# Optimization experiments

Hardware: AMD Instinct MI355X
Metric: run time of the kernel (lower is better)

## Reference

```python
import jax, jax.numpy as jnp
import numpy as np

D_MODEL = 1024
NHEAD = 16
HEAD_DIM = D_MODEL // NHEAD
SF_THRESHOLD = 4.0
SF_LEVELS = 8
SF_STEP = SF_THRESHOLD / SF_LEVELS  # 0.5
EPS = 1e-6


def sfn(x):
    # Scale-and-Fire neuron: quantize activations to multiples of SF_STEP,
    # clipped to +/- num_levels, with straight-through estimator.
    q = jnp.clip(jnp.round(x / SF_STEP), -SF_LEVELS, SF_LEVELS) * SF_STEP
    return x + jax.lax.stop_gradient(q - x)


def qk_norm(x, g):
    # RMS-normalize over the head_dim (last axis) with learnable gain g [Dh].
    rms = jnp.sqrt(jnp.mean(x * x, axis=-1, keepdims=True) + EPS)
    return (x / rms) * g


def setup_inputs() -> dict:
    key = jax.random.key(0)
    ks = jax.random.split(key, 10)
    B, L, D = 2, 2048, D_MODEL
    s = 1.0 / np.sqrt(D)
    return {
        "x": jax.random.normal(ks[0], (B, L, D), dtype=jnp.float32),
        "Wq": jax.random.normal(ks[1], (D, D), dtype=jnp.float32) * s,
        "bq": jnp.zeros((D,), dtype=jnp.float32),
        "Wk": jax.random.normal(ks[2], (D, D), dtype=jnp.float32) * s,
        "bk": jnp.zeros((D,), dtype=jnp.float32),
        "Wv": jax.random.normal(ks[3], (D, D), dtype=jnp.float32) * s,
        "bv": jnp.zeros((D,), dtype=jnp.float32),
        "Wo": jax.random.normal(ks[4], (D, D), dtype=jnp.float32) * s,
        "bo": jnp.zeros((D,), dtype=jnp.float32),
        "gq": jnp.ones((HEAD_DIM,), dtype=jnp.float32),
        "gk": jnp.ones((HEAD_DIM,), dtype=jnp.float32),
    }


def reference(x, Wq, bq, Wk, bk, Wv, bv, Wo, bo, gq, gk):
    B, L, D = x.shape
    H, Dh = NHEAD, HEAD_DIM
    scale = Dh ** (-0.5)

    q = sfn(x @ Wq.T + bq)
    k = sfn(x @ Wk.T + bk)
    v = sfn(x @ Wv.T + bv)

    # [B, L, H, Dh] -> [B, H, L, Dh]
    q = q.reshape(B, L, H, Dh).transpose(0, 2, 1, 3)
    k = k.reshape(B, L, H, Dh).transpose(0, 2, 1, 3)
    v = v.reshape(B, L, H, Dh).transpose(0, 2, 1, 3)

    q = qk_norm(q, gq)
    k = qk_norm(k, gk)

    scores = jnp.einsum('bhqd,bhkd->bhqk', q, k) * scale
    probs = jax.nn.softmax(scores, axis=-1)  # dropout is identity (eval)
    out = jnp.einsum('bhqk,bhkd->bhqd', probs, v)
    out = out.transpose(0, 2, 1, 3).reshape(B, L, D)
    return out @ Wo.T + bo
```

## Files before the change

kernel.cpp:

```cpp
#include <hip/hip_runtime.h>
#include <math.h>


typedef __bf16 bf16;
typedef bf16 bf16x4 __attribute__((ext_vector_type(4)));
typedef bf16 bf16x8 __attribute__((ext_vector_type(8)));
typedef float f32x4 __attribute__((ext_vector_type(4)));

#define LOG2E 1.4426950408889634f

__device__ __forceinline__ float sfn_f(float x) {
  return fminf(fmaxf(rintf(x + x), -8.0f), 8.0f) * 0.5f;
}

__device__ __forceinline__ void gload16(const bf16* g, bf16* l) {
  __builtin_amdgcn_global_load_lds((const __attribute__((address_space(1))) void*)g,
                                   (__attribute__((address_space(3))) void*)l, 16, 0, 0);
}


__global__ __launch_bounds__(256) void prep_x_kernel(const float* __restrict__ x,
                                                     bf16* __restrict__ ax) {
  int idx = blockIdx.x * 256 + threadIdx.x;
  int m  = idx >> 8;
  int kc = (idx & 255) << 2;
  const float4 v = *(const float4*)(x + (size_t)m * 1024 + kc);
  bf16 h0 = (bf16)v.x, h1 = (bf16)v.y, h2 = (bf16)v.z, h3 = (bf16)v.w;
  bf16 l0 = (bf16)(v.x - (float)h0), l1 = (bf16)(v.y - (float)h1),
       l2 = (bf16)(v.z - (float)h2), l3 = (bf16)(v.w - (float)h3);
  bf16x4 hv = {h0, h1, h2, h3};
  bf16x4 lv = {l0, l1, l2, l3};
  bf16* p = ax + (size_t)m * 3072 + kc;
  *(bf16x4*)(p)        = hv;
  *(bf16x4*)(p + 1024) = lv;
  *(bf16x4*)(p + 2048) = hv;
}

__global__ __launch_bounds__(256) void prep_w_kernel(const float* __restrict__ Wq,
                                                     const float* __restrict__ Wk,
                                                     const float* __restrict__ Wv,
                                                     bf16* __restrict__ wc) {
  int idx = blockIdx.x * 256 + threadIdx.x;
  int mat = idx >> 18;
  int r   = idx & 262143;
  int n   = r >> 8;
  int kc  = (r & 255) << 2;
  const float* W = (mat == 0) ? Wq : ((mat == 1) ? Wk : Wv);
  const float4 v = *(const float4*)(W + (size_t)n * 1024 + kc);
  bf16 h0 = (bf16)v.x, h1 = (bf16)v.y, h2 = (bf16)v.z, h3 = (bf16)v.w;
  bf16 l0 = (bf16)(v.x - (float)h0), l1 = (bf16)(v.y - (float)h1),
       l2 = (bf16)(v.z - (float)h2), l3 = (bf16)(v.w - (float)h3);
  bf16x4 hv = {h0, h1, h2, h3};
  bf16x4 lv = {l0, l1, l2, l3};
  bf16* p = wc + (size_t)(mat * 1024 + n) * 3072 + kc;
  *(bf16x4*)(p)        = hv;
  *(bf16x4*)(p + 1024) = hv;
  *(bf16x4*)(p + 2048) = lv;
}

__global__ __launch_bounds__(256) void prep_wo_kernel(const float* __restrict__ Wo,
                                                      bf16* __restrict__ wob) {
  int idx = blockIdx.x * 256 + threadIdx.x;
  const float4 v = *(const float4*)(Wo + (size_t)idx * 4);
  bf16x4 hv = {(bf16)v.x, (bf16)v.y, (bf16)v.z, (bf16)v.w};
  *(bf16x4*)(wob + (size_t)idx * 4) = hv;
}


template <int MODE>
__global__ __launch_bounds__(256, 3) void gemm_bt_kernel(
    const bf16* __restrict__ A, const bf16* __restrict__ Bm, int K,
    const float* __restrict__ b0, const float* __restrict__ b1,
    const float* __restrict__ b2, const float* __restrict__ g0,
    const float* __restrict__ g1, bf16* __restrict__ qn, bf16* __restrict__ kn,
    bf16* __restrict__ vt, float* __restrict__ outf) {
  __shared__ bf16 sA[128 * 32];
  __shared__ bf16 sB[128 * 32];
  const int tid  = threadIdx.x;
  const int wave = tid >> 6;
  const int lane = tid & 63;
  const int lm   = lane & 15;
  const int kg   = lane >> 4;
  const int nbx = gridDim.x;
  const int lid = blockIdx.x + nbx * blockIdx.y;
  const int cpx = (nbx << 5) >> 3;
  const int logical = (lid & 7) * cpx + (lid >> 3);
  const int m0 = (logical / nbx) << 7;
  const int n0 = (logical % nbx) << 7;
  const int wm = (wave >> 1) << 6;
  const int wn = (wave & 1) << 6;

  f32x4 acc[4][4] = {};

  for (int kt = 0; kt < K; kt += 32) {
    __syncthreads();
#pragma unroll
    for (int j = 0; j < 2; ++j) {
      const int i   = wave * 128 + j * 64 + lane;
      const int row = i >> 2;
      const int kc  = (i & 3) << 3;
      gload16(A  + (size_t)(m0 + row) * K + kt + kc, sA + i * 8);
      gload16(Bm + (size_t)(n0 + row) * K + kt + kc, sB + i * 8);
    }
    __syncthreads();
    bf16x8 af[4], bfv[4];
#pragma unroll
    for (int r = 0; r < 4; ++r)
      af[r] = *(const bf16x8*)(sA + (wm + 16 * r + lm) * 32 + kg * 8);
#pragma unroll
    for (int c = 0; c < 4; ++c)
      bfv[c] = *(const bf16x8*)(sB + (wn + 16 * c + lm) * 32 + kg * 8);
#pragma unroll
    for (int r = 0; r < 4; ++r)
#pragma unroll
      for (int c = 0; c < 4; ++c)
        acc[r][c] = __builtin_amdgcn_mfma_f32_16x16x32_bf16(af[r], bfv[c], acc[r][c], 0, 0, 0);
  }

  if (MODE == 0) {
    const int ncb = n0 + wn;
    const int mat = ncb >> 10;
    const int nin = ncb & 1023;
    const int hh  = nin >> 6;
    const float* bias = (mat == 0) ? b0 : ((mat == 1) ? b1 : b2);
    float bvals[4];
#pragma unroll
    for (int c = 0; c < 4; ++c) bvals[c] = bias[nin + 16 * c + lm];

    if (mat < 2) {
      const float* gain = (mat == 0) ? g0 : g1;
      bf16* dst = (mat == 0) ? qn : kn;
      float gv[4];
#pragma unroll
      for (int c = 0; c < 4; ++c) gv[c] = gain[16 * c + lm];
#pragma unroll
      for (int r = 0; r < 4; ++r) {
        float y[4][4];
        float ss[4] = {0.f, 0.f, 0.f, 0.f};
#pragma unroll
        for (int c = 0; c < 4; ++c)
#pragma unroll
          for (int g = 0; g < 4; ++g) {
            float t = sfn_f(acc[r][c][g] + bvals[c]);
            y[c][g] = t;
            ss[g] += t * t;
          }
#pragma unroll
        for (int g = 0; g < 4; ++g) {
          float s = ss[g];
          s += __shfl_xor(s, 1);
          s += __shfl_xor(s, 2);
          s += __shfl_xor(s, 4);
          s += __shfl_xor(s, 8);
          ss[g] = 1.0f / sqrtf(s * (1.0f / 64.0f) + 1e-6f);
        }
        const int mbase = m0 + wm + 16 * r + 4 * kg;
        const int bb = mbase >> 11;
        const int ll = mbase & 2047;
#pragma unroll
        for (int g = 0; g < 4; ++g) {
          bf16* rowp = dst + ((size_t)(bb * 16 + hh) * 2048 + (ll + g)) * 64;
#pragma unroll
          for (int c = 0; c < 4; ++c)
            rowp[16 * c + lm] = (bf16)(y[c][g] * ss[g] * gv[c]);
        }
      }
    } else {
#pragma unroll
      for (int r = 0; r < 4; ++r) {
        const int mbase = m0 + wm + 16 * r + 4 * kg;
        const int bb = mbase >> 11;
        const int ll = mbase & 2047;
#pragma unroll
        for (int c = 0; c < 4; ++c) {
          bf16x4 pk;
#pragma unroll
          for (int g = 0; g < 4; ++g)
            pk[g] = (bf16)sfn_f(acc[r][c][g] + bvals[c]);
          *(bf16x4*)(vt + ((size_t)(bb * 16 + hh) * 64 + 16 * c + lm) * 2048 + ll) = pk;
        }
      }
    }
  } else {
    float bvals[4];
#pragma unroll
    for (int c = 0; c < 4; ++c) bvals[c] = b0[n0 + wn + 16 * c + lm];
#pragma unroll
    for (int r = 0; r < 4; ++r) {
      const int mr = m0 + wm + 16 * r + 4 * kg;
#pragma unroll
      for (int c = 0; c < 4; ++c) {
        const int nc = n0 + wn + 16 * c + lm;
#pragma unroll
        for (int g = 0; g < 4; ++g)
          outf[(size_t)(mr + g) * 1024 + nc] = acc[r][c][g] + bvals[c];
      }
    }
  }
}


__global__ __launch_bounds__(256, 3) void attn_kernel(const bf16* __restrict__ qn,
                                                      const bf16* __restrict__ kn,
                                                      const bf16* __restrict__ vt,
                                                      bf16* __restrict__ ao) {
  __shared__ bf16 sK[2][64 * 64];
  __shared__ bf16 sV[2][64 * 64];
  __shared__ bf16 sP[4][16 * 72];
  const int tid  = threadIdx.x;
  const int wave = tid >> 6;
  const int lane = tid & 63;
  const int lm   = lane & 15;
  const int kg   = lane >> 4;
  const int lid     = blockIdx.x + (blockIdx.y << 4);
  const int logical = ((lid & 7) << 6) | (lid >> 3);
  const int qblk    = logical & 15;
  const int bh      = logical >> 4;
  const int q0      = (qblk << 7) + (wave << 5);
  const bf16* qb = qn + (size_t)bh * 2048 * 64;
  const bf16* kb = kn + (size_t)bh * 2048 * 64;
  const bf16* vb = vt + (size_t)bh * 64 * 2048;

  const float C1 = 0.125f * LOG2E;
  const float C2 = -8.0f * LOG2E;

  const int srow7 = lane >> 3;
  const int scl   = (lane & 7) ^ srow7;
  auto stage = [&](int buf, int kt) {
#pragma unroll
    for (int j = 0; j < 2; ++j) {
      const int ci  = wave * 2 + j;
      const int row = ci * 8 + srow7;
      gload16(kb + (size_t)(kt + row) * 64 + scl * 8, &sK[buf][ci * 512]);
      gload16(vb + (size_t)row * 2048 + kt + scl * 8, &sV[buf][ci * 512]);
    }
  };

  bf16x8 qf[2][2];
#pragma unroll
  for (int c = 0; c < 2; ++c)
#pragma unroll
    for (int dh = 0; dh < 2; ++dh)
      qf[c][dh] = *(const bf16x8*)(qb + (size_t)(q0 + 16 * c + lm) * 64 + dh * 32 + kg * 8);

  f32x4 o[4][2] = {};
  float lrun[2] = {0.f, 0.f};

  stage(0, 0);
  asm volatile("s_waitcnt vmcnt(0)" ::: "memory");
  __syncthreads();

  const int a7 = lm & 7;
  for (int t = 0; t < 32; ++t) {
    const int cur = t & 1;
    if (t < 31) stage(cur ^ 1, (t + 1) * 64);

    bf16x8 ka[4][2];
#pragma unroll
    for (int rb = 0; rb < 4; ++rb)
#pragma unroll
      for (int dh = 0; dh < 2; ++dh)
        ka[rb][dh] = *(const bf16x8*)(&sK[cur][(16 * rb + lm) * 64 + ((dh * 4 + kg) ^ a7) * 8]);

    f32x4 s[4][2] = {};
#pragma unroll
    for (int rb = 0; rb < 4; ++rb)
#pragma unroll
      for (int c = 0; c < 2; ++c)
#pragma unroll
        for (int dh = 0; dh < 2; ++dh)
          s[rb][c] = __builtin_amdgcn_mfma_f32_16x16x32_bf16(ka[rb][dh], qf[c][dh], s[rb][c], 0, 0, 0);

    bf16x8 pb[2][2];
#pragma unroll
    for (int c = 0; c < 2; ++c) {
#pragma unroll
      for (int rb = 0; rb < 4; ++rb) {
        bf16x4 pk;
#pragma unroll
        for (int g = 0; g < 4; ++g) {
          float p = __builtin_amdgcn_exp2f(fmaf(s[rb][c][g], C1, C2));
          lrun[c] += p;
          pk[g] = (bf16)p;
        }
        *(bf16x4*)(&sP[wave][lm * 72 + 16 * rb + 4 * kg]) = pk;
      }
      asm volatile("s_waitcnt lgkmcnt(0)" ::: "memory");
#pragma unroll
      for (int kh = 0; kh < 2; ++kh)
        pb[c][kh] = *(const bf16x8*)(&sP[wave][lm * 72 + kh * 32 + kg * 8]);
    }

    bf16x8 va[4][2];
#pragma unroll
    for (int rbd = 0; rbd < 4; ++rbd)
#pragma unroll
      for (int kh = 0; kh < 2; ++kh)
        va[rbd][kh] = *(const bf16x8*)(&sV[cur][(16 * rbd + lm) * 64 + ((kh * 4 + kg) ^ a7) * 8]);

#pragma unroll
    for (int rbd = 0; rbd < 4; ++rbd)
#pragma unroll
      for (int c = 0; c < 2; ++c)
#pragma unroll
        for (int kh = 0; kh < 2; ++kh)
          o[rbd][c] = __builtin_amdgcn_mfma_f32_16x16x32_bf16(va[rbd][kh], pb[c][kh], o[rbd][c], 0, 0, 0);

    asm volatile("s_waitcnt vmcnt(0)" ::: "memory");
    __syncthreads();
  }

  const int bb = bh >> 4;
  const int hh = bh & 15;
#pragma unroll
  for (int c = 0; c < 2; ++c) {
    float l = lrun[c];
    l += __shfl_xor(l, 16);
    l += __shfl_xor(l, 32);
    const float inv = 1.0f / l;
    const int q = q0 + 16 * c + lm;
    bf16* rowp = ao + (size_t)(bb * 2048 + q) * 1024 + hh * 64;
#pragma unroll
    for (int rbd = 0; rbd < 4; ++rbd) {
      bf16x4 pk;
#pragma unroll
      for (int g = 0; g < 4; ++g)
        pk[g] = (bf16)(o[rbd][c][g] * inv);
      *(bf16x4*)(rowp + 16 * rbd + 4 * kg) = pk;
    }
  }
}


extern "C" void kernel_launch(void* const* d_in, const int* in_sizes, int n_in,
                              void* d_out, int out_size, void* d_ws, size_t ws_size,
                              hipStream_t stream) {
  const float* x  = (const float*)d_in[0];
  const float* Wq = (const float*)d_in[1];
  const float* bq = (const float*)d_in[2];
  const float* Wk = (const float*)d_in[3];
  const float* bk = (const float*)d_in[4];
  const float* Wv = (const float*)d_in[5];
  const float* bv = (const float*)d_in[6];
  const float* Wo = (const float*)d_in[7];
  const float* bo = (const float*)d_in[8];
  const float* gq = (const float*)d_in[9];
  const float* gk = (const float*)d_in[10];
  float* out = (float*)d_out;

  char* ws = (char*)d_ws;
  bf16* ax   = (bf16*)(ws);
  bf16* wc   = (bf16*)(ws + 25165824);
  bf16* wob  = (bf16*)(ws + 44040192);
  bf16* qn   = (bf16*)(ws + 46137344);
  bf16* kn   = (bf16*)(ws + 54525952);
  bf16* vt   = (bf16*)(ws + 62914560);
  bf16* attn = (bf16*)(ws + 71303168);

  prep_x_kernel<<<dim3(4096), dim3(256), 0, stream>>>(x, ax);
  prep_w_kernel<<<dim3(3072), dim3(256), 0, stream>>>(Wq, Wk, Wv, wc);
  prep_wo_kernel<<<dim3(1024), dim3(256), 0, stream>>>(Wo, wob);

  gemm_bt_kernel<0><<<dim3(24, 32), dim3(256), 0, stream>>>(
      ax, wc, 3072, bq, bk, bv, gq, gk, qn, kn, vt, nullptr);

  attn_kernel<<<dim3(16, 32), dim3(256), 0, stream>>>(qn, kn, vt, attn);

  gemm_bt_kernel<1><<<dim3(8, 32), dim3(256), 0, stream>>>(
      attn, wob, 1024, bo, nullptr, nullptr, nullptr, nullptr,
      nullptr, nullptr, nullptr, out);
}
```

Measured before the change: 271.9 us.

## Rewrite QKV GEMM as 256x256 pipelined 8-wave kernel and split attention K/V staging

Replaces the QKV projection GEMM with a dedicated 512-thread kernel using 256x256 tiles and K=64 steps. It uses swizzled LDS, staggered half-tile prefetch with partial vmcnt waits, barrier-phased MFMA blocks and setprio. In attention, K and V loads are issued separately so V for the next tile streams in during the current QK step. P also gets a per-column buffer, which drops an intermediate lgkmcnt wait. The goal is more data reuse and better overlap of global loads with MFMA, at the cost of more LDS, more registers and fewer resident blocks.

```diff
diff --git a/kernel.cpp b/kernel.cpp
--- a/kernel.cpp
+++ b/kernel.cpp
@@ -8,6 +8,14 @@
 typedef float f32x4 __attribute__((ext_vector_type(4)));
 
 #define LOG2E 1.4426950408889634f
+#define MFMA16 __builtin_amdgcn_mfma_f32_16x16x32_bf16
+#define S_WAITV(N) asm volatile("s_waitcnt vmcnt(" #N ")" ::: "memory")
+
+__device__ __forceinline__ void bar() {
+  asm volatile("" ::: "memory");
+  __builtin_amdgcn_s_barrier();
+  asm volatile("" ::: "memory");
+}
 
 __device__ __forceinline__ float sfn_f(float x) {
   return fminf(fmaxf(rintf(x + x), -8.0f), 8.0f) * 0.5f;
@@ -67,13 +75,202 @@
 }
 
 
-template <int MODE>
-__global__ __launch_bounds__(256, 3) void gemm_bt_kernel(
-    const bf16* __restrict__ A, const bf16* __restrict__ Bm, int K,
+__global__ __launch_bounds__(512, 2) void gemm_qkv_kernel(
+    const bf16* __restrict__ A, const bf16* __restrict__ Bm,
     const float* __restrict__ b0, const float* __restrict__ b1,
     const float* __restrict__ b2, const float* __restrict__ g0,
     const float* __restrict__ g1, bf16* __restrict__ qn, bf16* __restrict__ kn,
-    bf16* __restrict__ vt, float* __restrict__ outf) {
+    bf16* __restrict__ vt) {
+  constexpr int K = 3072, NT = 48;
+  __shared__ bf16 lds[2][4][128 * 64];
+  const int tid  = threadIdx.x;
+  const int wave = tid >> 6;
+  const int lane = tid & 63;
+  const int lm   = lane & 15;
+  const int kg   = lane >> 4;
+  const int wm   = wave >> 2;
+  const int wn   = wave & 3;
+  const int lid     = blockIdx.x;
+  const int logical = (lid & 7) * 24 + (lid >> 3);
+  const int m0 = (logical / 12) << 8;
+  const int n0 = (logical % 12) << 8;
+
+  const bf16* Abase = A  + (size_t)m0 * K;
+  const bf16* Bbase = Bm + (size_t)n0 * K;
+
+  auto stageHalf = [&](int buf, int half, const bf16* base, int kt) {
+#pragma unroll
+    for (int j = 0; j < 2; ++j) {
+      const int c    = j * 512 + tid;
+      const int row  = c >> 3;
+      const int col8 = (c & 7) ^ (row & 7);
+      gload16(base + (size_t)row * K + kt + col8 * 8, &lds[buf][half][c * 8]);
+    }
+  };
+
+  f32x4 acc[8][4] = {};
+  const int bHalf = 2 + (wn >> 1);
+  const int bRow  = (wn & 1) << 6;
+  const int sw    = lm & 7;
+
+  stageHalf(0, 0, Abase, 0);
+  stageHalf(0, 1, Abase + (size_t)128 * K, 0);
+  stageHalf(0, 2, Bbase, 0);
+  stageHalf(0, 3, Bbase + (size_t)128 * K, 0);
+  stageHalf(1, 0, Abase, 64);
+  stageHalf(1, 1, Abase + (size_t)128 * K, 64);
+  S_WAITV(4);
+  bar();
+
+  for (int t = 0; t < NT; ++t) {
+    const int cur = t & 1, nxt = cur ^ 1;
+    const int kt1 = (t + 1) << 6;
+    bf16x8 a[4][2], p01[2][2], p23[2][2];
+#pragma unroll
+    for (int r = 0; r < 4; ++r)
+#pragma unroll
+      for (int kk = 0; kk < 2; ++kk)
+        a[r][kk] = *(const bf16x8*)&lds[cur][wm][(16 * r + lm) * 64 + (((kk << 2) + kg) ^ sw) * 8];
+#pragma unroll
+    for (int c = 0; c < 2; ++c)
+#pragma unroll
+      for (int kk = 0; kk < 2; ++kk)
+        p01[c][kk] = *(const bf16x8*)&lds[cur][bHalf][(bRow + 16 * c + lm) * 64 + (((kk << 2) + kg) ^ sw) * 8];
+    if (t + 1 < NT) stageHalf(nxt, 2, Bbase, kt1);
+    bar();
+    __builtin_amdgcn_s_setprio(1);
+#pragma unroll
+    for (int r = 0; r < 4; ++r)
+#pragma unroll
+      for (int c = 0; c < 2; ++c)
+#pragma unroll
+        for (int kk = 0; kk < 2; ++kk)
+          acc[r][c] = MFMA16(a[r][kk], p01[c][kk], acc[r][c], 0, 0, 0);
+    __builtin_amdgcn_s_setprio(0);
+    bar();
+#pragma unroll
+    for (int c = 0; c < 2; ++c)
+#pragma unroll
+      for (int kk = 0; kk < 2; ++kk)
+        p23[c][kk] = *(const bf16x8*)&lds[cur][bHalf][(bRow + 16 * (c + 2) + lm) * 64 + (((kk << 2) + kg) ^ sw) * 8];
+    if (t + 1 < NT) stageHalf(nxt, 3, Bbase + (size_t)128 * K, kt1);
+    bar();
+    __builtin_amdgcn_s_setprio(1);
+#pragma unroll
+    for (int r = 0; r < 4; ++r)
+#pragma unroll
+      for (int c = 0; c < 2; ++c)
+#pragma unroll
+        for (int kk = 0; kk < 2; ++kk)
+          acc[r][c + 2] = MFMA16(a[r][kk], p23[c][kk], acc[r][c + 2], 0, 0, 0);
+    __builtin_amdgcn_s_setprio(0);
+    bar();
+#pragma unroll
+    for (int r = 0; r < 4; ++r)
+#pragma unroll
+      for (int kk = 0; kk < 2; ++kk)
+        a[r][kk] = *(const bf16x8*)&lds[cur][wm][(64 + 16 * r + lm) * 64 + (((kk << 2) + kg) ^ sw) * 8];
+    bar();
+    __builtin_amdgcn_s_setprio(1);
+#pragma unroll
+    for (int r = 0; r < 4; ++r)
+#pragma unroll
+      for (int c = 0; c < 2; ++c)
+#pragma unroll
+        for (int kk = 0; kk < 2; ++kk)
+          acc[4 + r][c + 2] = MFMA16(a[r][kk], p23[c][kk], acc[4 + r][c + 2], 0, 0, 0);
+    __builtin_amdgcn_s_setprio(0);
+    bar();
+    if (t + 2 < NT) {
+      const int kt2 = (t + 2) << 6;
+      stageHalf(cur, 0, Abase, kt2);
+      stageHalf(cur, 1, Abase + (size_t)128 * K, kt2);
+      S_WAITV(4);
+    } else {
+      S_WAITV(0);
+    }
+    bar();
+    __builtin_amdgcn_s_setprio(1);
+#pragma unroll
+    for (int r = 0; r < 4; ++r)
+#pragma unroll
+      for (int c = 0; c < 2; ++c)
+#pragma unroll
+        for (int kk = 0; kk < 2; ++kk)
+          acc[4 + r][c] = MFMA16(a[r][kk], p01[c][kk], acc[4 + r][c], 0, 0, 0);
+    __builtin_amdgcn_s_setprio(0);
+    bar();
+  }
+
+  const int ncb = n0 + (wn << 6);
+  const int mat = ncb >> 10;
+  const int nin = ncb & 1023;
+  const int hh  = nin >> 6;
+  const float* bias = (mat == 0) ? b0 : ((mat == 1) ? b1 : b2);
+  float bvals[4];
+#pragma unroll
+  for (int c = 0; c < 4; ++c) bvals[c] = bias[nin + 16 * c + lm];
+
+  if (mat < 2) {
+    const float* gain = (mat == 0) ? g0 : g1;
+    bf16* dst = (mat == 0) ? qn : kn;
+    float gv[4];
+#pragma unroll
+    for (int c = 0; c < 4; ++c) gv[c] = gain[16 * c + lm];
+#pragma unroll
+    for (int r = 0; r < 8; ++r) {
+      float y[4][4];
+      float ss[4] = {0.f, 0.f, 0.f, 0.f};
+#pragma unroll
+      for (int c = 0; c < 4; ++c)
+#pragma unroll
+        for (int g = 0; g < 4; ++g) {
+          float tq = sfn_f(acc[r][c][g] + bvals[c]);
+          y[c][g] = tq;
+          ss[g] += tq * tq;
+        }
+#pragma unroll
+      for (int g = 0; g < 4; ++g) {
+        float s = ss[g];
+        s += __shfl_xor(s, 1);
+        s += __shfl_xor(s, 2);
+        s += __shfl_xor(s, 4);
+        s += __shfl_xor(s, 8);
+        ss[g] = 1.0f / sqrtf(s * (1.0f / 64.0f) + 1e-6f);
+      }
+      const int mbase = m0 + (wm << 7) + 16 * r + 4 * kg;
+      const int bb = mbase >> 11;
+      const int ll = mbase & 2047;
+#pragma unroll
+      for (int g = 0; g < 4; ++g) {
+        bf16* rowp = dst + ((size_t)(bb * 16 + hh) * 2048 + (ll + g)) * 64;
+#pragma unroll
+        for (int c = 0; c < 4; ++c)
+          rowp[16 * c + lm] = (bf16)(y[c][g] * ss[g] * gv[c]);
+      }
+    }
+  } else {
+#pragma unroll
+    for (int r = 0; r < 8; ++r) {
+      const int mbase = m0 + (wm << 7) + 16 * r + 4 * kg;
+      const int bb = mbase >> 11;
+      const int ll = mbase & 2047;
+#pragma unroll
+      for (int c = 0; c < 4; ++c) {
+        bf16x4 pk;
+#pragma unroll
+        for (int g = 0; g < 4; ++g)
+          pk[g] = (bf16)sfn_f(acc[r][c][g] + bvals[c]);
+        *(bf16x4*)(vt + ((size_t)(bb * 16 + hh) * 64 + 16 * c + lm) * 2048 + ll) = pk;
+      }
+    }
+  }
+}
+
+
+__global__ __launch_bounds__(256, 3) void gemm_o_kernel(
+    const bf16* __restrict__ A, const bf16* __restrict__ Bm, int K,
+    const float* __restrict__ b0, float* __restrict__ outf) {
   __shared__ bf16 sA[128 * 32];
   __shared__ bf16 sB[128 * 32];
   const int tid  = threadIdx.x;
@@ -114,87 +311,21 @@
     for (int r = 0; r < 4; ++r)
 #pragma unroll
       for (int c = 0; c < 4; ++c)
-        acc[r][c] = __builtin_amdgcn_mfma_f32_16x16x32_bf16(af[r], bfv[c], acc[r][c], 0, 0, 0);
+        acc[r][c] = MFMA16(af[r], bfv[c], acc[r][c], 0, 0, 0);
   }
 
-  if (MODE == 0) {
-    const int ncb = n0 + wn;
-    const int mat = ncb >> 10;
-    const int nin = ncb & 1023;
-    const int hh  = nin >> 6;
-    const float* bias = (mat == 0) ? b0 : ((mat == 1) ? b1 : b2);
-    float bvals[4];
-#pragma unroll
-    for (int c = 0; c < 4; ++c) bvals[c] = bias[nin + 16 * c + lm];
-
-    if (mat < 2) {
-      const float* gain = (mat == 0) ? g0 : g1;
-      bf16* dst = (mat == 0) ? qn : kn;
-      float gv[4];
-#pragma unroll
-      for (int c = 0; c < 4; ++c) gv[c] = gain[16 * c + lm];
-#pragma unroll
-      for (int r = 0; r < 4; ++r) {
-        float y[4][4];
-        float ss[4] = {0.f, 0.f, 0.f, 0.f};
-#pragma unroll
-        for (int c = 0; c < 4; ++c)
-#pragma unroll
-          for (int g = 0; g < 4; ++g) {
-            float t = sfn_f(acc[r][c][g] + bvals[c]);
-            y[c][g] = t;
-            ss[g] += t * t;
-          }
-#pragma unroll
-        for (int g = 0; g < 4; ++g) {
-          float s = ss[g];
-          s += __shfl_xor(s, 1);
-          s += __shfl_xor(s, 2);
-          s += __shfl_xor(s, 4);
-          s += __shfl_xor(s, 8);
-          ss[g] = 1.0f / sqrtf(s * (1.0f / 64.0f) + 1e-6f);
-        }
-        const int mbase = m0 + wm + 16 * r + 4 * kg;
-        const int bb = mbase >> 11;
-        const int ll = mbase & 2047;
-#pragma unroll
-        for (int g = 0; g < 4; ++g) {
-          bf16* rowp = dst + ((size_t)(bb * 16 + hh) * 2048 + (ll + g)) * 64;
-#pragma unroll
-          for (int c = 0; c < 4; ++c)
-            rowp[16 * c + lm] = (bf16)(y[c][g] * ss[g] * gv[c]);
-        }
-      }
-    } else {
-#pragma unroll
-      for (int r = 0; r < 4; ++r) {
-        const int mbase = m0 + wm + 16 * r + 4 * kg;
-        const int bb = mbase >> 11;
-        const int ll = mbase & 2047;
-#pragma unroll
-        for (int c = 0; c < 4; ++c) {
-          bf16x4 pk;
-#pragma unroll
-          for (int g = 0; g < 4; ++g)
-            pk[g] = (bf16)sfn_f(acc[r][c][g] + bvals[c]);
-          *(bf16x4*)(vt + ((size_t)(bb * 16 + hh) * 64 + 16 * c + lm) * 2048 + ll) = pk;
-        }
-      }
-    }
-  } else {
-    float bvals[4];
-#pragma unroll
-    for (int c = 0; c < 4; ++c) bvals[c] = b0[n0 + wn + 16 * c + lm];
-#pragma unroll
-    for (int r = 0; r < 4; ++r) {
-      const int mr = m0 + wm + 16 * r + 4 * kg;
-#pragma unroll
-      for (int c = 0; c < 4; ++c) {
-        const int nc = n0 + wn + 16 * c + lm;
-#pragma unroll
-        for (int g = 0; g < 4; ++g)
-          outf[(size_t)(mr + g) * 1024 + nc] = acc[r][c][g] + bvals[c];
-      }
+  float bvals[4];
+#pragma unroll
+  for (int c = 0; c < 4; ++c) bvals[c] = b0[n0 + wn + 16 * c + lm];
+#pragma unroll
+  for (int r = 0; r < 4; ++r) {
+    const int mr = m0 + wm + 16 * r + 4 * kg;
+#pragma unroll
+    for (int c = 0; c < 4; ++c) {
+      const int nc = n0 + wn + 16 * c + lm;
+#pragma unroll
+      for (int g = 0; g < 4; ++g)
+        outf[(size_t)(mr + g) * 1024 + nc] = acc[r][c][g] + bvals[c];
     }
   }
 }
@@ -206,7 +337,7 @@
                                                       bf16* __restrict__ ao) {
   __shared__ bf16 sK[2][64 * 64];
   __shared__ bf16 sV[2][64 * 64];
-  __shared__ bf16 sP[4][16 * 72];
+  __shared__ bf16 sP[4][2][16 * 72];
   const int tid  = threadIdx.x;
   const int wave = tid >> 6;
   const int lane = tid & 63;
@@ -226,12 +357,19 @@
 
   const int srow7 = lane >> 3;
   const int scl   = (lane & 7) ^ srow7;
-  auto stage = [&](int buf, int kt) {
+  auto stageK = [&](int buf, int kt) {
 #pragma unroll
     for (int j = 0; j < 2; ++j) {
       const int ci  = wave * 2 + j;
       const int row = ci * 8 + srow7;
       gload16(kb + (size_t)(kt + row) * 64 + scl * 8, &sK[buf][ci * 512]);
+    }
+  };
+  auto stageV = [&](int buf, int kt) {
+#pragma unroll
+    for (int j = 0; j < 2; ++j) {
+      const int ci  = wave * 2 + j;
+      const int row = ci * 8 + srow7;
       gload16(vb + (size_t)row * 2048 + kt + scl * 8, &sV[buf][ci * 512]);
     }
   };
@@ -246,14 +384,16 @@
   f32x4 o[4][2] = {};
   float lrun[2] = {0.f, 0.f};
 
-  stage(0, 0);
-  asm volatile("s_waitcnt vmcnt(0)" ::: "memory");
-  __syncthreads();
+  stageK(0, 0);
+  stageV(0, 0);
+  S_WAITV(0);
+  bar();
 
   const int a7 = lm & 7;
   for (int t = 0; t < 32; ++t) {
-    const int cur = t & 1;
-    if (t < 31) stage(cur ^ 1, (t + 1) * 64);
+    const int cur = t & 1, nxt = cur ^ 1;
+    const int ktn = (t + 1) << 6;
+    if (t < 31) stageK(nxt, ktn);
 
     bf16x8 ka[4][2];
 #pragma unroll
@@ -263,17 +403,20 @@
         ka[rb][dh] = *(const bf16x8*)(&sK[cur][(16 * rb + lm) * 64 + ((dh * 4 + kg) ^ a7) * 8]);
 
     f32x4 s[4][2] = {};
+    __builtin_amdgcn_s_setprio(1);
 #pragma unroll
     for (int rb = 0; rb < 4; ++rb)
 #pragma unroll
       for (int c = 0; c < 2; ++c)
 #pragma unroll
         for (int dh = 0; dh < 2; ++dh)
-          s[rb][c] = __builtin_amdgcn_mfma_f32_16x16x32_bf16(ka[rb][dh], qf[c][dh], s[rb][c], 0, 0, 0);
-
-    bf16x8 pb[2][2];
-#pragma unroll
-    for (int c = 0; c < 2; ++c) {
+          s[rb][c] = MFMA16(ka[rb][dh], qf[c][dh], s[rb][c], 0, 0, 0);
+    __builtin_amdgcn_s_setprio(0);
+
+    if (t < 31) stageV(nxt, ktn);
+
+#pragma unroll
+    for (int c = 0; c < 2; ++c)
 #pragma unroll
       for (int rb = 0; rb < 4; ++rb) {
         bf16x4 pk;
@@ -283,13 +426,17 @@
           lrun[c] += p;
           pk[g] = (bf16)p;
         }
-        *(bf16x4*)(&sP[wave][lm * 72 + 16 * rb + 4 * kg]) = pk;
+        *(bf16x4*)(&sP[wave][c][lm * 72 + 16 * rb + 4 * kg]) = pk;
       }
-      asm volatile("s_waitcnt lgkmcnt(0)" ::: "memory");
+    bf16x8 pb[2][2];
+#pragma unroll
+    for (int c = 0; c < 2; ++c)
 #pragma unroll
       for (int kh = 0; kh < 2; ++kh)
-        pb[c][kh] = *(const bf16x8*)(&sP[wave][lm * 72 + kh * 32 + kg * 8]);
-    }
+        pb[c][kh] = *(const bf16x8*)(&sP[wave][c][lm * 72 + kh * 32 + kg * 8]);
+
+    if (t < 31) { S_WAITV(4); } else { S_WAITV(0); }
+    bar();
 
     bf16x8 va[4][2];
 #pragma unroll
@@ -298,16 +445,20 @@
       for (int kh = 0; kh < 2; ++kh)
         va[rbd][kh] = *(const bf16x8*)(&sV[cur][(16 * rbd + lm) * 64 + ((kh * 4 + kg) ^ a7) * 8]);
 
+    __builtin_amdgcn_s_setprio(1);
 #pragma unroll
     for (int rbd = 0; rbd < 4; ++rbd)
 #pragma unroll
       for (int c = 0; c < 2; ++c)
 #pragma unroll
         for (int kh = 0; kh < 2; ++kh)
-          o[rbd][c] = __builtin_amdgcn_mfma_f32_16x16x32_bf16(va[rbd][kh], pb[c][kh], o[rbd][c], 0, 0, 0);
-
-    asm volatile("s_waitcnt vmcnt(0)" ::: "memory");
-    __syncthreads();
+          o[rbd][c] = MFMA16(va[rbd][kh], pb[c][kh], o[rbd][c], 0, 0, 0);
+    __builtin_amdgcn_s_setprio(0);
+
+    if (t < 31) {
+      S_WAITV(2);
+      bar();
+    }
   }
 
   const int bb = bh >> 4;
@@ -361,12 +512,11 @@
   prep_w_kernel<<<dim3(3072), dim3(256), 0, stream>>>(Wq, Wk, Wv, wc);
   prep_wo_kernel<<<dim3(1024), dim3(256), 0, stream>>>(Wo, wob);
 
-  gemm_bt_kernel<0><<<dim3(24, 32), dim3(256), 0, stream>>>(
-      ax, wc, 3072, bq, bk, bv, gq, gk, qn, kn, vt, nullptr);
+  gemm_qkv_kernel<<<dim3(192), dim3(512), 0, stream>>>(
+      ax, wc, bq, bk, bv, gq, gk, qn, kn, vt);
 
   attn_kernel<<<dim3(16, 32), dim3(256), 0, stream>>>(qn, kn, vt, attn);
 
-  gemm_bt_kernel<1><<<dim3(8, 32), dim3(256), 0, stream>>>(
-      attn, wob, 1024, bo, nullptr, nullptr, nullptr, nullptr,
-      nullptr, nullptr, nullptr, out);
-}
+  gemm_o_kernel<<<dim3(8, 32), dim3(256), 0, stream>>>(
+      attn, wob, 1024, bo, out);
+}
```

New measurement: 260.4 us. 1.04x faster.

## Retile QKV GEMM to 256x192 with 12 waves and load attention K/V into registers

Applied to the files above, without the earlier changes.

The fused QKV projection GEMM moves to a dedicated kernel with 768-thread blocks and 256x192 output tiles. It uses a K-step of 64, XOR-swizzled LDS double buffering and s_setprio around MFMA bursts. This raises operand reuse per LDS load and cuts the block count to one wave of 256 blocks. The attention kernel drops LDS staging of K/V and loads them straight from global memory into registers, ping-ponging two tiles to overlap loads with MFMA. That removes barriers but adds register pressure, so its occupancy hint falls to 2.

```diff
diff --git a/kernel.cpp b/kernel.cpp
--- a/kernel.cpp
+++ b/kernel.cpp
@@ -8,6 +8,14 @@
 typedef float f32x4 __attribute__((ext_vector_type(4)));
 
 #define LOG2E 1.4426950408889634f
+#define MFMA16 __builtin_amdgcn_mfma_f32_16x16x32_bf16
+#define S_WAITV(N) asm volatile("s_waitcnt vmcnt(" #N ")" ::: "memory")
+
+__device__ __forceinline__ void bar() {
+  asm volatile("" ::: "memory");
+  __builtin_amdgcn_s_barrier();
+  asm volatile("" ::: "memory");
+}
 
 __device__ __forceinline__ float sfn_f(float x) {
   return fminf(fmaxf(rintf(x + x), -8.0f), 8.0f) * 0.5f;
@@ -67,13 +75,163 @@
 }
 
 
-template <int MODE>
-__global__ __launch_bounds__(256, 3) void gemm_bt_kernel(
-    const bf16* __restrict__ A, const bf16* __restrict__ Bm, int K,
+__global__ __launch_bounds__(768, 3) void gemm_qkv_kernel(
+    const bf16* __restrict__ A, const bf16* __restrict__ Bm,
     const float* __restrict__ b0, const float* __restrict__ b1,
     const float* __restrict__ b2, const float* __restrict__ g0,
     const float* __restrict__ g1, bf16* __restrict__ qn, bf16* __restrict__ kn,
-    bf16* __restrict__ vt, float* __restrict__ outf) {
+    bf16* __restrict__ vt) {
+  constexpr int K = 3072, NT = 48;
+  __shared__ bf16 lds[2][3584 * 8];
+  const int tid  = threadIdx.x;
+  const int wave = tid >> 6;
+  const int lane = tid & 63;
+  const int lm   = lane & 15;
+  const int kg   = lane >> 4;
+  const int wmr  = wave & 3;
+  const int wnc  = wave >> 2;
+  const int lid     = blockIdx.x;
+  const int logical = ((lid & 7) << 5) | (lid >> 3);
+  const int m0 = (logical >> 4) << 8;
+  const int n0 = (logical & 15) * 192;
+
+  auto stage = [&](int buf, int kt) {
+#pragma unroll
+    for (int j = 0; j < 5; ++j) {
+      const int i = tid + j * 768;
+      if (i < 3584) {
+        if (i < 2048) {
+          const int row  = i >> 3;
+          const int col8 = (i & 7) ^ (row & 7);
+          gload16(A + (size_t)(m0 + row) * K + kt + col8 * 8, &lds[buf][i * 8]);
+        } else {
+          const int i2   = i - 2048;
+          const int row  = i2 >> 3;
+          const int col8 = (i2 & 7) ^ (row & 7);
+          gload16(Bm + (size_t)(n0 + row) * K + kt + col8 * 8, &lds[buf][i * 8]);
+        }
+      }
+    }
+  };
+
+  auto rdA = [&](int buf, int r, int kk) -> bf16x8 {
+    const int row = (wmr << 6) + (r << 4) + lm;
+    return *(const bf16x8*)&lds[buf][(row * 8 + (((kk << 2) + kg) ^ (row & 7))) * 8];
+  };
+  auto rdB = [&](int buf, int c, int kk) -> bf16x8 {
+    const int row = (wnc << 6) + (c << 4) + lm;
+    return *(const bf16x8*)&lds[buf][(2048 * 8) + (row * 8 + (((kk << 2) + kg) ^ (row & 7))) * 8];
+  };
+
+  f32x4 acc[4][4] = {};
+
+  stage(0, 0);
+  S_WAITV(0);
+  bar();
+
+  for (int t = 0; t < NT; ++t) {
+    const int cur = t & 1;
+    if (t + 1 < NT) stage(cur ^ 1, (t + 1) << 6);
+
+    bf16x8 a0[4], bq0[4];
+#pragma unroll
+    for (int r = 0; r < 4; ++r) a0[r] = rdA(cur, r, 0);
+#pragma unroll
+    for (int c = 0; c < 4; ++c) bq0[c] = rdB(cur, c, 0);
+    __builtin_amdgcn_s_setprio(1);
+#pragma unroll
+    for (int r = 0; r < 4; ++r)
+#pragma unroll
+      for (int c = 0; c < 4; ++c)
+        acc[r][c] = MFMA16(a0[r], bq0[c], acc[r][c], 0, 0, 0);
+    __builtin_amdgcn_s_setprio(0);
+
+    bf16x8 a1[4], bq1[4];
+#pragma unroll
+    for (int r = 0; r < 4; ++r) a1[r] = rdA(cur, r, 1);
+#pragma unroll
+    for (int c = 0; c < 4; ++c) bq1[c] = rdB(cur, c, 1);
+    __builtin_amdgcn_s_setprio(1);
+#pragma unroll
+    for (int r = 0; r < 4; ++r)
+#pragma unroll
+      for (int c = 0; c < 4; ++c)
+        acc[r][c] = MFMA16(a1[r], bq1[c], acc[r][c], 0, 0, 0);
+    __builtin_amdgcn_s_setprio(0);
+
+    S_WAITV(0);
+    bar();
+  }
+
+  const int gcol = n0 + (wnc << 6);
+  const int mat  = gcol >> 10;
+  const int cb   = gcol & 1023;
+  const int hh   = cb >> 6;
+  const float* bias = (mat == 0) ? b0 : ((mat == 1) ? b1 : b2);
+  float bvals[4];
+#pragma unroll
+  for (int j = 0; j < 4; ++j) bvals[j] = bias[cb + 16 * j + lm];
+
+  if (mat < 2) {
+    const float* gain = (mat == 0) ? g0 : g1;
+    bf16* dst = (mat == 0) ? qn : kn;
+    float gv[4];
+#pragma unroll
+    for (int j = 0; j < 4; ++j) gv[j] = gain[16 * j + lm];
+#pragma unroll
+    for (int r = 0; r < 4; ++r) {
+      float y[4][4];
+      float ss[4] = {0.f, 0.f, 0.f, 0.f};
+#pragma unroll
+      for (int j = 0; j < 4; ++j)
+#pragma unroll
+        for (int g = 0; g < 4; ++g) {
+          float tq = sfn_f(acc[r][j][g] + bvals[j]);
+          y[j][g] = tq;
+          ss[g] += tq * tq;
+        }
+#pragma unroll
+      for (int g = 0; g < 4; ++g) {
+        float s = ss[g];
+        s += __shfl_xor(s, 1);
+        s += __shfl_xor(s, 2);
+        s += __shfl_xor(s, 4);
+        s += __shfl_xor(s, 8);
+        ss[g] = 1.0f / sqrtf(s * (1.0f / 64.0f) + 1e-6f);
+      }
+      const int mbase = m0 + (wmr << 6) + 16 * r + 4 * kg;
+      const int bb = mbase >> 11;
+      const int ll = mbase & 2047;
+#pragma unroll
+      for (int g = 0; g < 4; ++g) {
+        bf16* rowp = dst + ((size_t)(bb * 16 + hh) * 2048 + (ll + g)) * 64;
+#pragma unroll
+        for (int j = 0; j < 4; ++j)
+          rowp[16 * j + lm] = (bf16)(y[j][g] * ss[g] * gv[j]);
+      }
+    }
+  } else {
+#pragma unroll
+    for (int r = 0; r < 4; ++r) {
+      const int mbase = m0 + (wmr << 6) + 16 * r + 4 * kg;
+      const int bb = mbase >> 11;
+      const int ll = mbase & 2047;
+#pragma unroll
+      for (int j = 0; j < 4; ++j) {
+        bf16x4 pk;
+#pragma unroll
+        for (int g = 0; g < 4; ++g)
+          pk[g] = (bf16)sfn_f(acc[r][j][g] + bvals[j]);
+        *(bf16x4*)(vt + ((size_t)(bb * 16 + hh) * 64 + 16 * j + lm) * 2048 + ll) = pk;
+      }
+    }
+  }
+}
+
+
+__global__ __launch_bounds__(256, 3) void gemm_o_kernel(
+    const bf16* __restrict__ A, const bf16* __restrict__ Bm, int K,
+    const float* __restrict__ b0, float* __restrict__ outf) {
   __shared__ bf16 sA[128 * 32];
   __shared__ bf16 sB[128 * 32];
   const int tid  = threadIdx.x;
@@ -114,98 +272,30 @@
     for (int r = 0; r < 4; ++r)
 #pragma unroll
       for (int c = 0; c < 4; ++c)
-        acc[r][c] = __builtin_amdgcn_mfma_f32_16x16x32_bf16(af[r], bfv[c], acc[r][c], 0, 0, 0);
-  }
-
-  if (MODE == 0) {
-    const int ncb = n0 + wn;
-    const int mat = ncb >> 10;
-    const int nin = ncb & 1023;
-    const int hh  = nin >> 6;
-    const float* bias = (mat == 0) ? b0 : ((mat == 1) ? b1 : b2);
-    float bvals[4];
-#pragma unroll
-    for (int c = 0; c < 4; ++c) bvals[c] = bias[nin + 16 * c + lm];
-
-    if (mat < 2) {
-      const float* gain = (mat == 0) ? g0 : g1;
-      bf16* dst = (mat == 0) ? qn : kn;
-      float gv[4];
-#pragma unroll
-      for (int c = 0; c < 4; ++c) gv[c] = gain[16 * c + lm];
-#pragma unroll
-      for (int r = 0; r < 4; ++r) {
-        float y[4][4];
-        float ss[4] = {0.f, 0.f, 0.f, 0.f};
-#pragma unroll
-        for (int c = 0; c < 4; ++c)
-#pragma unroll
-          for (int g = 0; g < 4; ++g) {
-            float t = sfn_f(acc[r][c][g] + bvals[c]);
-            y[c][g] = t;
-            ss[g] += t * t;
-          }
-#pragma unroll
-        for (int g = 0; g < 4; ++g) {
-          float s = ss[g];
-          s += __shfl_xor(s, 1);
-          s += __shfl_xor(s, 2);
-          s += __shfl_xor(s, 4);
-          s += __shfl_xor(s, 8);
-          ss[g] = 1.0f / sqrtf(s * (1.0f / 64.0f) + 1e-6f);
-        }
-        const int mbase = m0 + wm + 16 * r + 4 * kg;
-        const int bb = mbase >> 11;
-        const int ll = mbase & 2047;
-#pragma unroll
-        for (int g = 0; g < 4; ++g) {
-          bf16* rowp = dst + ((size_t)(bb * 16 + hh) * 2048 + (ll + g)) * 64;
-#pragma unroll
-          for (int c = 0; c < 4; ++c)
-            rowp[16 * c + lm] = (bf16)(y[c][g] * ss[g] * gv[c]);
-        }
-      }
-    } else {
-#pragma unroll
-      for (int r = 0; r < 4; ++r) {
-        const int mbase = m0 + wm + 16 * r + 4 * kg;
-        const int bb = mbase >> 11;
-        const int ll = mbase & 2047;
-#pragma unroll
-        for (int c = 0; c < 4; ++c) {
-          bf16x4 pk;
-#pragma unroll
-          for (int g = 0; g < 4; ++g)
-            pk[g] = (bf16)sfn_f(acc[r][c][g] + bvals[c]);
-          *(bf16x4*)(vt + ((size_t)(bb * 16 + hh) * 64 + 16 * c + lm) * 2048 + ll) = pk;
-        }
-      }
-    }
-  } else {
-    float bvals[4];
-#pragma unroll
-    for (int c = 0; c < 4; ++c) bvals[c] = b0[n0 + wn + 16 * c + lm];
-#pragma unroll
-    for (int r = 0; r < 4; ++r) {
-      const int mr = m0 + wm + 16 * r + 4 * kg;
-#pragma unroll
-      for (int c = 0; c < 4; ++c) {
-        const int nc = n0 + wn + 16 * c + lm;
-#pragma unroll
-        for (int g = 0; g < 4; ++g)
-          outf[(size_t)(mr + g) * 1024 + nc] = acc[r][c][g] + bvals[c];
-      }
-    }
-  }
-}
-
-
-__global__ __launch_bounds__(256, 3) void attn_kernel(const bf16* __restrict__ qn,
+        acc[r][c] = MFMA16(af[r], bfv[c], acc[r][c], 0, 0, 0);
+  }
+
+  float bvals[4];
+#pragma unroll
+  for (int c = 0; c < 4; ++c) bvals[c] = b0[n0 + wn + 16 * c + lm];
+#pragma unroll
+  for (int r = 0; r < 4; ++r) {
+    const int mr = m0 + wm + 16 * r + 4 * kg;
+#pragma unroll
+    for (int c = 0; c < 4; ++c) {
+      const int nc = n0 + wn + 16 * c + lm;
+#pragma unroll
+      for (int g = 0; g < 4; ++g)
+        outf[(size_t)(mr + g) * 1024 + nc] = acc[r][c][g] + bvals[c];
+    }
+  }
+}
+
+
+__global__ __launch_bounds__(256, 2) void attn_kernel(const bf16* __restrict__ qn,
                                                       const bf16* __restrict__ kn,
                                                       const bf16* __restrict__ vt,
                                                       bf16* __restrict__ ao) {
-  __shared__ bf16 sK[2][64 * 64];
-  __shared__ bf16 sV[2][64 * 64];
   __shared__ bf16 sP[4][16 * 72];
   const int tid  = threadIdx.x;
   const int wave = tid >> 6;
@@ -224,18 +314,6 @@
   const float C1 = 0.125f * LOG2E;
   const float C2 = -8.0f * LOG2E;
 
-  const int srow7 = lane >> 3;
-  const int scl   = (lane & 7) ^ srow7;
-  auto stage = [&](int buf, int kt) {
-#pragma unroll
-    for (int j = 0; j < 2; ++j) {
-      const int ci  = wave * 2 + j;
-      const int row = ci * 8 + srow7;
-      gload16(kb + (size_t)(kt + row) * 64 + scl * 8, &sK[buf][ci * 512]);
-      gload16(vb + (size_t)row * 2048 + kt + scl * 8, &sV[buf][ci * 512]);
-    }
-  };
-
   bf16x8 qf[2][2];
 #pragma unroll
   for (int c = 0; c < 2; ++c)
@@ -246,30 +324,32 @@
   f32x4 o[4][2] = {};
   float lrun[2] = {0.f, 0.f};
 
-  stage(0, 0);
-  asm volatile("s_waitcnt vmcnt(0)" ::: "memory");
-  __syncthreads();
-
-  const int a7 = lm & 7;
-  for (int t = 0; t < 32; ++t) {
-    const int cur = t & 1;
-    if (t < 31) stage(cur ^ 1, (t + 1) * 64);
-
-    bf16x8 ka[4][2];
+  auto loadK = [&](bf16x8 (&ka)[4][2], int kt) {
 #pragma unroll
     for (int rb = 0; rb < 4; ++rb)
 #pragma unroll
       for (int dh = 0; dh < 2; ++dh)
-        ka[rb][dh] = *(const bf16x8*)(&sK[cur][(16 * rb + lm) * 64 + ((dh * 4 + kg) ^ a7) * 8]);
-
+        ka[rb][dh] = *(const bf16x8*)(kb + (size_t)(kt + 16 * rb + lm) * 64 + dh * 32 + kg * 8);
+  };
+  auto loadV = [&](bf16x8 (&va)[4][2], int kt) {
+#pragma unroll
+    for (int rbd = 0; rbd < 4; ++rbd)
+#pragma unroll
+      for (int kh = 0; kh < 2; ++kh)
+        va[rbd][kh] = *(const bf16x8*)(vb + (size_t)(16 * rbd + lm) * 2048 + kt + kh * 32 + kg * 8);
+  };
+
+  auto tile = [&](const bf16x8 (&ka)[4][2], const bf16x8 (&va)[4][2]) {
     f32x4 s[4][2] = {};
+    __builtin_amdgcn_s_setprio(1);
 #pragma unroll
     for (int rb = 0; rb < 4; ++rb)
 #pragma unroll
       for (int c = 0; c < 2; ++c)
 #pragma unroll
         for (int dh = 0; dh < 2; ++dh)
-          s[rb][c] = __builtin_amdgcn_mfma_f32_16x16x32_bf16(ka[rb][dh], qf[c][dh], s[rb][c], 0, 0, 0);
+          s[rb][c] = MFMA16(ka[rb][dh], qf[c][dh], s[rb][c], 0, 0, 0);
+    __builtin_amdgcn_s_setprio(0);
 
     bf16x8 pb[2][2];
 #pragma unroll
@@ -291,23 +371,29 @@
         pb[c][kh] = *(const bf16x8*)(&sP[wave][lm * 72 + kh * 32 + kg * 8]);
     }
 
-    bf16x8 va[4][2];
+    __builtin_amdgcn_s_setprio(1);
 #pragma unroll
     for (int rbd = 0; rbd < 4; ++rbd)
 #pragma unroll
-      for (int kh = 0; kh < 2; ++kh)
-        va[rbd][kh] = *(const bf16x8*)(&sV[cur][(16 * rbd + lm) * 64 + ((kh * 4 + kg) ^ a7) * 8]);
-
-#pragma unroll
-    for (int rbd = 0; rbd < 4; ++rbd)
-#pragma unroll
       for (int c = 0; c < 2; ++c)
 #pragma unroll
         for (int kh = 0; kh < 2; ++kh)
-          o[rbd][c] = __builtin_amdgcn_mfma_f32_16x16x32_bf16(va[rbd][kh], pb[c][kh], o[rbd][c], 0, 0, 0);
-
-    asm volatile("s_waitcnt vmcnt(0)" ::: "memory");
-    __syncthreads();
+          o[rbd][c] = MFMA16(va[rbd][kh], pb[c][kh], o[rbd][c], 0, 0, 0);
+    __builtin_amdgcn_s_setprio(0);
+  };
+
+  bf16x8 kA[4][2], vA[4][2], kB[4][2], vB[4][2];
+  loadK(kA, 0);
+  loadV(vA, 0);
+  for (int t = 0; t < 32; t += 2) {
+    loadK(kB, (t + 1) << 6);
+    loadV(vB, (t + 1) << 6);
+    tile(kA, vA);
+    if (t + 2 < 32) {
+      loadK(kA, (t + 2) << 6);
+      loadV(vA, (t + 2) << 6);
+    }
+    tile(kB, vB);
   }
 
   const int bb = bh >> 4;
@@ -361,12 +447,11 @@
   prep_w_kernel<<<dim3(3072), dim3(256), 0, stream>>>(Wq, Wk, Wv, wc);
   prep_wo_kernel<<<dim3(1024), dim3(256), 0, stream>>>(Wo, wob);
 
-  gemm_bt_kernel<0><<<dim3(24, 32), dim3(256), 0, stream>>>(
-      ax, wc, 3072, bq, bk, bv, gq, gk, qn, kn, vt, nullptr);
+  gemm_qkv_kernel<<<dim3(256), dim3(768), 0, stream>>>(
+      ax, wc, bq, bk, bv, gq, gk, qn, kn, vt);
 
   attn_kernel<<<dim3(16, 32), dim3(256), 0, stream>>>(qn, kn, vt, attn);
 
-  gemm_bt_kernel<1><<<dim3(8, 32), dim3(256), 0, stream>>>(
-      attn, wob, 1024, bo, nullptr, nullptr, nullptr, nullptr,
-      nullptr, nullptr, nullptr, out);
-}
+  gemm_o_kernel<<<dim3(8, 32), dim3(256), 0, stream>>>(
+      attn, wob, 1024, bo, out);
+}
```

Result: slower. 305.4 us (+12.3%).
